# Kernel tuning notes

Hardware: AMD Instinct MI355X
Metric: run time of the kernel (lower is better)

The kernel has to match this reference:

```python
import jax, jax.numpy as jnp
import numpy as np

B = 32768      # number of sets
N = 131072     # total elements
DIM = 128      # feature dim
HID = 64       # hidden dim
MAXP = 17      # max_n + 1 (one-hot positional dim / size-class count)


def _ln(x, g, b, eps=1e-5):
    m = jnp.mean(x, -1, keepdims=True)
    v = jnp.var(x, -1, keepdims=True)
    return (x - m) * jax.lax.rsqrt(v + eps) * g + b


def _mlp_ln(x, w1, b1, g, bt, w2, b2):
    return jnp.tanh(_ln(x @ w1 + b1, g, bt)) @ w2 + b2


def _mlp(x, w1, b1, w2, b2):
    return jnp.tanh(x @ w1 + b1) @ w2 + b2


def _lin_init(key, fan_in, fan_out):
    k1, k2 = jax.random.split(key)
    s = 1.0 / np.sqrt(fan_in)
    return (jax.random.uniform(k1, (fan_in, fan_out), jnp.float32, -s, s),
            jax.random.uniform(k2, (fan_out,), jnp.float32, -s, s))


def setup_inputs() -> dict:
    key = jax.random.key(0)
    ks = jax.random.split(key, 16)
    inp = {}
    inp['x'] = jax.random.normal(ks[0], (N, DIM), jnp.float32)
    inp['batch'] = jnp.sort(jax.random.randint(ks[1], (N,), 0, B)).astype(jnp.int64)
    # rank: Linear(dim, 1)
    inp['rank_w'], inp['rank_b'] = _lin_init(ks[2], DIM, 1)
    # enc_psi: dim -> 96 -> hid, LayerNorm
    inp['psi_w1'], inp['psi_b1'] = _lin_init(ks[3], DIM, 96)
    inp['psi_g'] = jnp.ones((96,), jnp.float32); inp['psi_bt'] = jnp.zeros((96,), jnp.float32)
    inp['psi_w2'], inp['psi_b2'] = _lin_init(ks[4], 96, HID)
    # encoder pos_encoder: 17 -> 40 -> hid, LayerNorm
    inp['pe_e_w1'], inp['pe_e_b1'] = _lin_init(ks[5], MAXP, 40)
    inp['pe_e_g'] = jnp.ones((40,), jnp.float32); inp['pe_e_bt'] = jnp.zeros((40,), jnp.float32)
    inp['pe_e_w2'], inp['pe_e_b2'] = _lin_init(ks[6], 40, HID)
    # enc_phi: (hid+17)=81 -> 72 -> hid, no LN
    inp['phi_w1'], inp['phi_b1'] = _lin_init(ks[7], HID + MAXP, 72)
    inp['phi_w2'], inp['phi_b2'] = _lin_init(ks[8], 72, HID)
    # size_pred: hid -> 40 -> 17, no LN
    inp['size_w1'], inp['size_b1'] = _lin_init(ks[9], HID, 40)
    inp['size_w2'], inp['size_b2'] = _lin_init(ks[10], 40, MAXP)
    # decoder pos_encoder: 17 -> 40 -> hid, LayerNorm
    inp['pe_d_w1'], inp['pe_d_b1'] = _lin_init(ks[11], MAXP, 40)
    inp['pe_d_g'] = jnp.ones((40,), jnp.float32); inp['pe_d_bt'] = jnp.zeros((40,), jnp.float32)
    inp['pe_d_w2'], inp['pe_d_b2'] = _lin_init(ks[12], 40, HID)
    # decoder: hid -> 96 -> dim, no LN
    inp['dec_w1'], inp['dec_b1'] = _lin_init(ks[13], HID, 96)
    inp['dec_w2'], inp['dec_b2'] = _lin_init(ks[14], 96, DIM)
    return inp


def reference(x, batch, rank_w, rank_b,
              psi_w1, psi_b1, psi_g, psi_bt, psi_w2, psi_b2,
              pe_e_w1, pe_e_b1, pe_e_g, pe_e_bt, pe_e_w2, pe_e_b2,
              phi_w1, phi_b1, phi_w2, phi_b2,
              size_w1, size_b1, size_w2, size_b2,
              pe_d_w1, pe_d_b1, pe_d_g, pe_d_bt, pe_d_w2, pe_d_b2,
              dec_w1, dec_b1, dec_w2, dec_b2):
    batch = batch.astype(jnp.int32)
    # ---- Encoder ----
    n = jax.ops.segment_sum(jnp.ones(N, jnp.int32), batch, num_segments=B)  # [B]
    seg_start = jnp.cumsum(n) - n                                           # ptr[:-1]
    mag = (x @ rank_w + rank_b).reshape(-1)                                 # rank scores
    idx = jnp.lexsort((mag, batch))  # per-segment sort (batch is grouped/sorted)
    xs = x[idx]                                                             # [N, DIM]
    keys = jnp.arange(N) - seg_start[batch]                                 # position in set
    pos = jax.nn.one_hot(keys, MAXP, dtype=x.dtype)                         # [N, MAXP]
    y1 = _mlp_ln(xs, psi_w1, psi_b1, psi_g, psi_bt, psi_w2, psi_b2) * \
         _mlp_ln(pos, pe_e_w1, pe_e_b1, pe_e_g, pe_e_bt, pe_e_w2, pe_e_b2)
    y2 = jax.ops.segment_sum(y1, batch, num_segments=B)                     # [B, HID]
    pos_n = jax.nn.one_hot(n, MAXP, dtype=x.dtype)
    z = _mlp(jnp.concatenate([y2, pos_n], -1), phi_w1, phi_b1, phi_w2, phi_b2)  # [B, HID]
    # ---- Decoder ----
    logits = _mlp(z, size_w1, size_b1, size_w2, size_b2)                    # [B, MAXP]
    n_dec = jnp.argmax(logits, -1)                                          # [B]
    pe = _mlp_ln(jnp.eye(MAXP, dtype=x.dtype),
                 pe_d_w1, pe_d_b1, pe_d_g, pe_d_bt, pe_d_w2, pe_d_b2)       # [MAXP, HID]
    zp = z[:, None, :] * pe[None, :, :]                                     # [B, MAXP, HID]
    xr = _mlp(zp, dec_w1, dec_b1, dec_w2, dec_b2)                           # [B, MAXP, DIM]
    mask = jnp.arange(MAXP)[None, :] < n_dec[:, None]                       # valid slots
    xr = jnp.where(mask[..., None], xr, 0.0)
    batchr = jnp.broadcast_to(jnp.arange(B)[:, None], (B, MAXP))
    return xr.reshape(B * MAXP, DIM), batchr.reshape(-1), mask.reshape(-1)
```

## Files before the change

### kernel.cpp

```cpp
#include <hip/hip_runtime.h>

#define NELEM 131072
#define BSETS 32768
#define DIM 128
#define HID 64
#define MAXP 17

typedef __attribute__((ext_vector_type(8))) short short8;
typedef __attribute__((ext_vector_type(4))) float f32x4;

__device__ __forceinline__ unsigned short f2bf(float f) {
  unsigned u = __float_as_uint(f);
  u += 0x7fff + ((u >> 16) & 1);
  return (unsigned short)(u >> 16);
}

__device__ void pos_mlp40(int row, const float* w1, const float* b1, const float* g,
                          const float* bt, const float* w2, const float* b2, float* out) {
  float h[40];
  for (int j = 0; j < 40; ++j) h[j] = b1[j] + (row >= 0 ? w1[row * 40 + j] : 0.0f);
  float s = 0.f;
  for (int j = 0; j < 40; ++j) s += h[j];
  float mean = s * (1.0f / 40.0f);
  float v = 0.f;
  for (int j = 0; j < 40; ++j) { float d = h[j] - mean; v += d * d; }
  float rs = rsqrtf(v * (1.0f / 40.0f) + 1e-5f);
  float tb[40];
  for (int j = 0; j < 40; ++j) tb[j] = tanhf((h[j] - mean) * rs * g[j] + bt[j]);
  for (int o = 0; o < 64; ++o) {
    float a = b2[o];
    for (int j = 0; j < 40; ++j) a += tb[j] * w2[j * 64 + o];
    out[o] = a;
  }
}

__global__ __launch_bounds__(256) void k_init(
    const float* __restrict__ x, const int* __restrict__ batch,
    const float* __restrict__ rank_w, const float* __restrict__ rank_b,
    double* __restrict__ mag, int* __restrict__ start,
    const float* ew1, const float* eb1, const float* eg, const float* ebt,
    const float* ew2, const float* eb2,
    const float* dw1, const float* db1, const float* dg, const float* dbt,
    const float* dw2, const float* db2,
    float* enc_tab, float* dec_tab,
    const float* __restrict__ decw1, const float* __restrict__ decw2,
    unsigned short* __restrict__ w1s, unsigned short* __restrict__ w2s) {
  int blk = blockIdx.x;
  int t = threadIdx.x;
  if (blk < 1024) {
    int lane = t & 63;
    int w = t >> 6;
    float2 wv = ((const float2*)rank_w)[lane];
    double w0 = wv.x, w1 = wv.y;
    double rb = rank_b[0];
    int rowbase = (blk * 4 + w) * 32;
    for (int it = 0; it < 32; ++it) {
      int row = rowbase + it;
      float2 xv = ((const float2*)(x + (size_t)row * DIM))[lane];
      double acc = (double)xv.x * w0 + (double)xv.y * w1;
#pragma unroll
      for (int m = 1; m < 64; m <<= 1)
        acc += __shfl_xor(acc, m, 64);
      if (lane == 0) mag[row] = acc + rb;
    }
  } else if (blk < 1536) {
    int i = (blk - 1024) * 256 + t;
    int b = batch[i];
    if (i == 0) {
      for (int bb = 0; bb <= b; ++bb) start[bb] = 0;
    } else {
      int bp = batch[i - 1];
      for (int bb = bp + 1; bb <= b; ++bb) start[bb] = i;
    }
    if (i == NELEM - 1) {
      for (int bb = b + 1; bb <= BSETS; ++bb) start[bb] = NELEM;
    }
  } else if (blk == 1536) {
    if (t < 18) {
      float out[64];
      pos_mlp40(t < 17 ? t : -1, ew1, eb1, eg, ebt, ew2, eb2, out);
      for (int o = 0; o < 64; ++o) enc_tab[t * 64 + o] = out[o];
    } else if (t >= 32 && t < 49) {
      float out[64];
      pos_mlp40(t - 32, dw1, db1, dg, dbt, dw2, db2, out);
      for (int o = 0; o < 64; ++o) dec_tab[(t - 32) * 64 + o] = out[o];
    }
  } else {
    int idx = (blk - 1537) * 256 + t;
    if (idx < 6144) {
      int i = idx & 7, lane = (idx >> 3) & 63, rest = idx >> 9;
      int jt = rest % 6, s = rest / 6;
      int k = s * 32 + (lane >> 4) * 8 + i;
      int n = jt * 16 + (lane & 15);
      w1s[idx] = f2bf(decw1[k * 96 + n]);
    }
    int idx2 = idx - 6144;
    if (idx2 >= 0 && idx2 < 12288) {
      int i = idx2 & 7, lane = (idx2 >> 3) & 63, rest = idx2 >> 9;
      int jt = rest % 8, s = rest / 8;
      int k = s * 32 + (lane >> 4) * 8 + i;
      int n = jt * 16 + (lane & 15);
      w2s[idx2] = f2bf(decw2[k * 128 + n]);
    }
  }
}

__global__ __launch_bounds__(256) void k_rank(const int* __restrict__ batch,
                                              const int* __restrict__ start,
                                              const double* __restrict__ mag,
                                              int* __restrict__ key) {
  int i = blockIdx.x * 256 + threadIdx.x;
  int b = batch[i];
  int s = start[b], e = start[b + 1];
  double mi = mag[i];
  int r = 0;
  for (int j = s; j < e; ++j) {
    double mj = mag[j];
    r += (mj < mi) || (mj == mi && j < i);
  }
  key[i] = r;
}

__global__ __launch_bounds__(256) void k_encoder(
    const float* __restrict__ x, const int* __restrict__ batch,
    const int* __restrict__ key, const int* __restrict__ start,
    const float* __restrict__ w1, const float* __restrict__ b1,
    const float* __restrict__ g, const float* __restrict__ bt,
    const float* __restrict__ w2, const float* __restrict__ b2,
    const float* __restrict__ enc_tab, float* __restrict__ y1) {
  __shared__ float xt[64][129];
  __shared__ float tt[64][97];
  __shared__ float ps1[4][64];
  __shared__ float ps2[4][64];
  int t = threadIdx.x;
  int base = blockIdx.x * 64;
  const float4* xg = (const float4*)(x + (size_t)base * DIM);
#pragma unroll
  for (int v = 0; v < 8; ++v) {
    int f = t + 256 * v;
    float4 val = xg[f];
    int e = f >> 5, kq = (f & 31) * 4;
    xt[e][kq] = val.x; xt[e][kq + 1] = val.y; xt[e][kq + 2] = val.z; xt[e][kq + 3] = val.w;
  }
  __syncthreads();
  int lane = t & 63;
  int w = __builtin_amdgcn_readfirstlane(t >> 6);
  int j0 = w * 24;
  float acc[24];
#pragma unroll
  for (int jj = 0; jj < 24; ++jj) acc[jj] = b1[j0 + jj];
  for (int k = 0; k < DIM; ++k) {
    float xv = xt[lane][k];
#pragma unroll
    for (int jj = 0; jj < 24; ++jj) acc[jj] += xv * w1[k * 96 + j0 + jj];
  }
  float s1 = 0.f, s2 = 0.f;
#pragma unroll
  for (int jj = 0; jj < 24; ++jj) { s1 += acc[jj]; s2 += acc[jj] * acc[jj]; }
  ps1[w][lane] = s1; ps2[w][lane] = s2;
  __syncthreads();
  float S1 = ps1[0][lane] + ps1[1][lane] + ps1[2][lane] + ps1[3][lane];
  float S2 = ps2[0][lane] + ps2[1][lane] + ps2[2][lane] + ps2[3][lane];
  float mean = S1 * (1.0f / 96.0f);
  float var = S2 * (1.0f / 96.0f) - mean * mean;
  float rs = rsqrtf(var + 1e-5f);
#pragma unroll
  for (int jj = 0; jj < 24; ++jj) {
    float hv = (acc[jj] - mean) * rs * g[j0 + jj] + bt[j0 + jj];
    tt[lane][j0 + jj] = tanhf(hv);
  }
  __syncthreads();
  int o0 = w * 16;
  float acc2[16];
#pragma unroll
  for (int oo = 0; oo < 16; ++oo) acc2[oo] = b2[o0 + oo];
  for (int j = 0; j < 96; ++j) {
    float tv = tt[lane][j];
#pragma unroll
    for (int oo = 0; oo < 16; ++oo) acc2[oo] += tv * w2[j * 64 + o0 + oo];
  }
  int gi = base + lane;
  int kk = key[gi];
  int row = kk < MAXP ? kk : MAXP;
  int bb = batch[gi];
  int pos = start[bb] + kk;
  const float* pe = enc_tab + row * 64;
#pragma unroll
  for (int oo = 0; oo < 16; ++oo) acc2[oo] *= pe[o0 + oo];
  float4* d4 = (float4*)(y1 + (size_t)pos * 64 + o0);
#pragma unroll
  for (int q = 0; q < 4; ++q)
    d4[q] = make_float4(acc2[4 * q], acc2[4 * q + 1], acc2[4 * q + 2], acc2[4 * q + 3]);
}

__global__ __launch_bounds__(256) void k_phi(const float* __restrict__ y1,
                                             const int* __restrict__ start,
                                             const float* __restrict__ w1, const float* __restrict__ b1,
                                             const float* __restrict__ w2, const float* __restrict__ b2,
                                             const float* __restrict__ sw1, const float* __restrict__ sb1,
                                             const float* __restrict__ sw2, const float* __restrict__ sb2,
                                             float* __restrict__ z, int* __restrict__ ndec) {
  __shared__ float yt[64][65];
  __shared__ float tt[64][73];
  __shared__ float zt[64][65];
  __shared__ float st[64][41];
  int t = threadIdx.x;
  int base = blockIdx.x * 64;
  {
    int s = t >> 2, c = t & 3;
    int sb = base + s;
    int ps = start[sb], pe = start[sb + 1];
    float acc[16];
#pragma unroll
    for (int i = 0; i < 16; ++i) acc[i] = 0.f;
    for (int p = ps; p < pe; ++p) {
      const float4* row = (const float4*)(y1 + (size_t)p * 64 + c * 16);
#pragma unroll
      for (int q = 0; q < 4; ++q) {
        float4 v = row[q];
        acc[4 * q] += v.x; acc[4 * q + 1] += v.y; acc[4 * q + 2] += v.z; acc[4 * q + 3] += v.w;
      }
    }
#pragma unroll
    for (int i = 0; i < 16; ++i) yt[s][c * 16 + i] = acc[i];
  }
  __syncthreads();
  int lane = t & 63;
  int w = __builtin_amdgcn_readfirstlane(t >> 6);
  int sb = base + lane;
  int nb = start[sb + 1] - start[sb];
  int j0 = w * 18;
  float acc[18];
#pragma unroll
  for (int jj = 0; jj < 18; ++jj) acc[jj] = b1[j0 + jj];
  for (int k = 0; k < 64; ++k) {
    float yv = yt[lane][k];
#pragma unroll
    for (int jj = 0; jj < 18; ++jj) acc[jj] += yv * w1[k * 72 + j0 + jj];
  }
  if (nb < MAXP) {
    const float* wr = w1 + (64 + nb) * 72 + j0;
#pragma unroll
    for (int jj = 0; jj < 18; ++jj) acc[jj] += wr[jj];
  }
#pragma unroll
  for (int jj = 0; jj < 18; ++jj) tt[lane][j0 + jj] = tanhf(acc[jj]);
  __syncthreads();
  int o0 = w * 16;
  float acc2[16];
#pragma unroll
  for (int oo = 0; oo < 16; ++oo) acc2[oo] = b2[o0 + oo];
  for (int j = 0; j < 72; ++j) {
    float tv = tt[lane][j];
#pragma unroll
    for (int oo = 0; oo < 16; ++oo) acc2[oo] += tv * w2[j * 64 + o0 + oo];
  }
  float4* zd = (float4*)(z + (size_t)sb * 64 + o0);
#pragma unroll
  for (int q = 0; q < 4; ++q)
    zd[q] = make_float4(acc2[4 * q], acc2[4 * q + 1], acc2[4 * q + 2], acc2[4 * q + 3]);
#pragma unroll
  for (int oo = 0; oo < 16; ++oo) zt[lane][o0 + oo] = acc2[oo];
  __syncthreads();
  int s0 = w * 10;
  float hs[10];
#pragma unroll
  for (int jj = 0; jj < 10; ++jj) hs[jj] = sb1[s0 + jj];
  for (int o = 0; o < 64; ++o) {
    float v = zt[lane][o];
#pragma unroll
    for (int jj = 0; jj < 10; ++jj) hs[jj] += v * sw1[o * 40 + s0 + jj];
  }
#pragma unroll
  for (int jj = 0; jj < 10; ++jj) st[lane][s0 + jj] = tanhf(hs[jj]);
  __syncthreads();
  if (w == 0) {
    float lg[17];
#pragma unroll
    for (int l = 0; l < 17; ++l) lg[l] = sb2[l];
    for (int j = 0; j < 40; ++j) {
      float tv = st[lane][j];
#pragma unroll
      for (int l = 0; l < 17; ++l) lg[l] += tv * sw2[j * 17 + l];
    }
    float best = lg[0]; int bi = 0;
#pragma unroll
    for (int l = 1; l < 17; ++l) if (lg[l] > best) { best = lg[l]; bi = l; }
    ndec[sb] = bi;
  }
}

__global__ __launch_bounds__(256) void k_decoder(
    const float* __restrict__ z, const float* __restrict__ dec_tab,
    const unsigned short* __restrict__ w1s, const unsigned short* __restrict__ w2s,
    const float* __restrict__ b1, const float* __restrict__ b2,
    const int* __restrict__ ndec, float* __restrict__ out0,
    float* __restrict__ out1, float* __restrict__ out2) {
  __shared__ __align__(16) unsigned short h2[64][104];
  int t = threadIdx.x;
  int lane = t & 63;
  int w = __builtin_amdgcn_readfirstlane(t >> 6);
  int quad = lane >> 4, m = lane & 15;
  int r = blockIdx.x * 64 + w * 16 + m;
  int b = r / 17, p = r - b * 17;
  const float* zr = z + (size_t)b * 64;
  const float* per = dec_tab + p * 64;
  short8 a1[2];
#pragma unroll
  for (int s = 0; s < 2; ++s) {
    int k0 = s * 32 + quad * 8;
#pragma unroll
    for (int i = 0; i < 8; ++i) {
      float v = zr[k0 + i] * per[k0 + i];
      ((unsigned short*)&a1[s])[i] = f2bf(v);
    }
  }
  const short8* w1f = (const short8*)w1s;
  f32x4 acc[6] = {};
#pragma unroll
  for (int jt = 0; jt < 6; ++jt) {
    acc[jt] = __builtin_amdgcn_mfma_f32_16x16x32_bf16(a1[0], w1f[jt * 64 + lane], acc[jt], 0, 0, 0);
    acc[jt] = __builtin_amdgcn_mfma_f32_16x16x32_bf16(a1[1], w1f[(6 + jt) * 64 + lane], acc[jt], 0, 0, 0);
  }
#pragma unroll
  for (int jt = 0; jt < 6; ++jt) {
    int col = jt * 16 + m;
    float bias = b1[col];
#pragma unroll
    for (int reg = 0; reg < 4; ++reg) {
      int rl = w * 16 + quad * 4 + reg;
      h2[rl][col] = f2bf(tanhf(acc[jt][reg] + bias));
    }
  }
  __syncthreads();
  short8 a2[3];
#pragma unroll
  for (int s = 0; s < 3; ++s)
    a2[s] = *(const short8*)&h2[w * 16 + m][s * 32 + quad * 8];
  const short8* w2f = (const short8*)w2s;
  f32x4 acc2[8] = {};
#pragma unroll
  for (int nt = 0; nt < 8; ++nt) {
#pragma unroll
    for (int s = 0; s < 3; ++s)
      acc2[nt] = __builtin_amdgcn_mfma_f32_16x16x32_bf16(a2[s], w2f[(s * 8 + nt) * 64 + lane], acc2[nt], 0, 0, 0);
  }
#pragma unroll
  for (int nt = 0; nt < 8; ++nt) {
    int n = nt * 16 + m;
    float bias = b2[n];
#pragma unroll
    for (int reg = 0; reg < 4; ++reg) {
      int rl = w * 16 + quad * 4 + reg;
      int rg = blockIdx.x * 64 + rl;
      int bb = rg / 17, pp = rg - bb * 17;
      float v = acc2[nt][reg] + bias;
      if (pp >= ndec[bb]) v = 0.0f;
      out0[(size_t)rg * 128 + n] = v;
    }
  }
  if (t < 64) {
    int rg = blockIdx.x * 64 + t;
    int bb = rg / 17, pp = rg - bb * 17;
    out1[rg] = (float)bb;
    out2[rg] = (pp < ndec[bb]) ? 1.0f : 0.0f;
  }
}

extern "C" void kernel_launch(void* const* d_in, const int* in_sizes, int n_in,
                              void* d_out, int out_size, void* d_ws, size_t ws_size,
                              hipStream_t stream) {
  const float* x = (const float*)d_in[0];
  const int* batch = (const int*)d_in[1];
  const float* rank_w = (const float*)d_in[2];
  const float* rank_b = (const float*)d_in[3];
  const float* psi_w1 = (const float*)d_in[4];
  const float* psi_b1 = (const float*)d_in[5];
  const float* psi_g = (const float*)d_in[6];
  const float* psi_bt = (const float*)d_in[7];
  const float* psi_w2 = (const float*)d_in[8];
  const float* psi_b2 = (const float*)d_in[9];
  const float* pe_e_w1 = (const float*)d_in[10];
  const float* pe_e_b1 = (const float*)d_in[11];
  const float* pe_e_g = (const float*)d_in[12];
  const float* pe_e_bt = (const float*)d_in[13];
  const float* pe_e_w2 = (const float*)d_in[14];
  const float* pe_e_b2 = (const float*)d_in[15];
  const float* phi_w1 = (const float*)d_in[16];
  const float* phi_b1 = (const float*)d_in[17];
  const float* phi_w2 = (const float*)d_in[18];
  const float* phi_b2 = (const float*)d_in[19];
  const float* size_w1 = (const float*)d_in[20];
  const float* size_b1 = (const float*)d_in[21];
  const float* size_w2 = (const float*)d_in[22];
  const float* size_b2 = (const float*)d_in[23];
  const float* pe_d_w1 = (const float*)d_in[24];
  const float* pe_d_b1 = (const float*)d_in[25];
  const float* pe_d_g = (const float*)d_in[26];
  const float* pe_d_bt = (const float*)d_in[27];
  const float* pe_d_w2 = (const float*)d_in[28];
  const float* pe_d_b2 = (const float*)d_in[29];
  const float* dec_w1 = (const float*)d_in[30];
  const float* dec_b1 = (const float*)d_in[31];
  const float* dec_w2 = (const float*)d_in[32];
  const float* dec_b2 = (const float*)d_in[33];

  char* ws = (char*)d_ws;
  int* start = (int*)(ws);
  double* mag = (double*)(ws + 0x40000);
  int* key = (int*)(ws + 0x140000);
  float* enc_tab = (float*)(ws + 0x1C0000);
  float* dec_tab = (float*)(ws + 0x1C2000);
  unsigned short* w1s = (unsigned short*)(ws + 0x1C4000);
  unsigned short* w2s = (unsigned short*)(ws + 0x1C8000);
  float* zbuf = (float*)(ws + 0x200000);
  int* ndec = (int*)(ws + 0xA00000);

  float* out0 = (float*)d_out;
  float* out1 = out0 + 71303168;
  float* out2 = out1 + 557056;

  float* y1 = out0;

  k_init<<<1609, 256, 0, stream>>>(x, batch, rank_w, rank_b, mag, start,
                                   pe_e_w1, pe_e_b1, pe_e_g, pe_e_bt, pe_e_w2, pe_e_b2,
                                   pe_d_w1, pe_d_b1, pe_d_g, pe_d_bt, pe_d_w2, pe_d_b2,
                                   enc_tab, dec_tab, dec_w1, dec_w2, w1s, w2s);
  k_rank<<<512, 256, 0, stream>>>(batch, start, mag, key);
  k_encoder<<<2048, 256, 0, stream>>>(x, batch, key, start, psi_w1, psi_b1, psi_g, psi_bt,
                                      psi_w2, psi_b2, enc_tab, y1);
  k_phi<<<512, 256, 0, stream>>>(y1, start, phi_w1, phi_b1, phi_w2, phi_b2,
                                 size_w1, size_b1, size_w2, size_b2, zbuf, ndec);
  k_decoder<<<8704, 256, 0, stream>>>(zbuf, dec_tab, w1s, w2s, dec_b1, dec_b2, ndec,
                                      out0, out1, out2);
}
```

Baseline: 652.8 us.

## Fuse rank into encoder, use fast tanh, vectorize decoder input loads

Removes the separate k_rank launch and computes each element's within-set rank inside k_encoder, overlapping it with the x tile load and dropping the key buffer round trip. Replaces tanhf everywhere with an exp/reciprocal approximation. Merges the encoder's two shared-memory tiles into one aliased buffer to cut LDS use. Vectorizes the decoder's z*pe input loads with float4. The approximate tanh may change results slightly, and the exp form could give NaN for large inputs where exp overflows.

```diff
diff --git a/kernel.cpp b/kernel.cpp
--- a/kernel.cpp
+++ b/kernel.cpp
@@ -13,6 +13,12 @@
   unsigned u = __float_as_uint(f);
   u += 0x7fff + ((u >> 16) & 1);
   return (unsigned short)(u >> 16);
+}
+
+__device__ __forceinline__ float fast_tanh(float x) {
+  float t = __expf(2.0f * x);
+  float r = __builtin_amdgcn_rcpf(t + 1.0f);
+  return fmaf(-2.0f, r, 1.0f);
 }
 
 __device__ void pos_mlp40(int row, const float* w1, const float* b1, const float* g,
@@ -26,7 +32,7 @@
   for (int j = 0; j < 40; ++j) { float d = h[j] - mean; v += d * d; }
   float rs = rsqrtf(v * (1.0f / 40.0f) + 1e-5f);
   float tb[40];
-  for (int j = 0; j < 40; ++j) tb[j] = tanhf((h[j] - mean) * rs * g[j] + bt[j]);
+  for (int j = 0; j < 40; ++j) tb[j] = fast_tanh((h[j] - mean) * rs * g[j] + bt[j]);
   for (int o = 0; o < 64; ++o) {
     float a = b2[o];
     for (int j = 0; j < 40; ++j) a += tb[j] * w2[j * 64 + o];
@@ -105,31 +111,14 @@
   }
 }
 
-__global__ __launch_bounds__(256) void k_rank(const int* __restrict__ batch,
-                                              const int* __restrict__ start,
-                                              const double* __restrict__ mag,
-                                              int* __restrict__ key) {
-  int i = blockIdx.x * 256 + threadIdx.x;
-  int b = batch[i];
-  int s = start[b], e = start[b + 1];
-  double mi = mag[i];
-  int r = 0;
-  for (int j = s; j < e; ++j) {
-    double mj = mag[j];
-    r += (mj < mi) || (mj == mi && j < i);
-  }
-  key[i] = r;
-}
-
 __global__ __launch_bounds__(256) void k_encoder(
     const float* __restrict__ x, const int* __restrict__ batch,
-    const int* __restrict__ key, const int* __restrict__ start,
+    const double* __restrict__ mag, const int* __restrict__ start,
     const float* __restrict__ w1, const float* __restrict__ b1,
     const float* __restrict__ g, const float* __restrict__ bt,
     const float* __restrict__ w2, const float* __restrict__ b2,
     const float* __restrict__ enc_tab, float* __restrict__ y1) {
-  __shared__ float xt[64][129];
-  __shared__ float tt[64][97];
+  __shared__ float sm[64 * 129];
   __shared__ float ps1[4][64];
   __shared__ float ps2[4][64];
   int t = threadIdx.x;
@@ -140,17 +129,27 @@
     int f = t + 256 * v;
     float4 val = xg[f];
     int e = f >> 5, kq = (f & 31) * 4;
-    xt[e][kq] = val.x; xt[e][kq + 1] = val.y; xt[e][kq + 2] = val.z; xt[e][kq + 3] = val.w;
-  }
-  __syncthreads();
+    float* xr = sm + e * 129 + kq;
+    xr[0] = val.x; xr[1] = val.y; xr[2] = val.z; xr[3] = val.w;
+  }
   int lane = t & 63;
   int w = __builtin_amdgcn_readfirstlane(t >> 6);
+  int gi = base + lane;
+  int bseg = batch[gi];
+  int segs = start[bseg], sege = start[bseg + 1];
+  double mi = mag[gi];
+  int kk = 0;
+  for (int j = segs; j < sege; ++j) {
+    double mj = mag[j];
+    kk += (mj < mi) || (mj == mi && j < gi);
+  }
+  __syncthreads();
   int j0 = w * 24;
   float acc[24];
 #pragma unroll
   for (int jj = 0; jj < 24; ++jj) acc[jj] = b1[j0 + jj];
   for (int k = 0; k < DIM; ++k) {
-    float xv = xt[lane][k];
+    float xv = sm[lane * 129 + k];
 #pragma unroll
     for (int jj = 0; jj < 24; ++jj) acc[jj] += xv * w1[k * 96 + j0 + jj];
   }
@@ -167,7 +166,7 @@
 #pragma unroll
   for (int jj = 0; jj < 24; ++jj) {
     float hv = (acc[jj] - mean) * rs * g[j0 + jj] + bt[j0 + jj];
-    tt[lane][j0 + jj] = tanhf(hv);
+    sm[lane * 97 + j0 + jj] = fast_tanh(hv);
   }
   __syncthreads();
   int o0 = w * 16;
@@ -175,15 +174,12 @@
 #pragma unroll
   for (int oo = 0; oo < 16; ++oo) acc2[oo] = b2[o0 + oo];
   for (int j = 0; j < 96; ++j) {
-    float tv = tt[lane][j];
+    float tv = sm[lane * 97 + j];
 #pragma unroll
     for (int oo = 0; oo < 16; ++oo) acc2[oo] += tv * w2[j * 64 + o0 + oo];
   }
-  int gi = base + lane;
-  int kk = key[gi];
   int row = kk < MAXP ? kk : MAXP;
-  int bb = batch[gi];
-  int pos = start[bb] + kk;
+  int pos = segs + kk;
   const float* pe = enc_tab + row * 64;
 #pragma unroll
   for (int oo = 0; oo < 16; ++oo) acc2[oo] *= pe[o0 + oo];
@@ -244,7 +240,7 @@
     for (int jj = 0; jj < 18; ++jj) acc[jj] += wr[jj];
   }
 #pragma unroll
-  for (int jj = 0; jj < 18; ++jj) tt[lane][j0 + jj] = tanhf(acc[jj]);
+  for (int jj = 0; jj < 18; ++jj) tt[lane][j0 + jj] = fast_tanh(acc[jj]);
   __syncthreads();
   int o0 = w * 16;
   float acc2[16];
@@ -272,7 +268,7 @@
     for (int jj = 0; jj < 10; ++jj) hs[jj] += v * sw1[o * 40 + s0 + jj];
   }
 #pragma unroll
-  for (int jj = 0; jj < 10; ++jj) st[lane][s0 + jj] = tanhf(hs[jj]);
+  for (int jj = 0; jj < 10; ++jj) st[lane][s0 + jj] = fast_tanh(hs[jj]);
   __syncthreads();
   if (w == 0) {
     float lg[17];
@@ -303,17 +299,19 @@
   int quad = lane >> 4, m = lane & 15;
   int r = blockIdx.x * 64 + w * 16 + m;
   int b = r / 17, p = r - b * 17;
-  const float* zr = z + (size_t)b * 64;
-  const float* per = dec_tab + p * 64;
+  const float4* z4 = (const float4*)(z + (size_t)b * 64);
+  const float4* p4 = (const float4*)(dec_tab + p * 64);
   short8 a1[2];
 #pragma unroll
   for (int s = 0; s < 2; ++s) {
-    int k0 = s * 32 + quad * 8;
-#pragma unroll
-    for (int i = 0; i < 8; ++i) {
-      float v = zr[k0 + i] * per[k0 + i];
-      ((unsigned short*)&a1[s])[i] = f2bf(v);
-    }
+    int q0 = (s * 32 + quad * 8) >> 2;
+    float4 za = z4[q0], zb = z4[q0 + 1];
+    float4 pa = p4[q0], pb = p4[q0 + 1];
+    unsigned short* ap = (unsigned short*)&a1[s];
+    ap[0] = f2bf(za.x * pa.x); ap[1] = f2bf(za.y * pa.y);
+    ap[2] = f2bf(za.z * pa.z); ap[3] = f2bf(za.w * pa.w);
+    ap[4] = f2bf(zb.x * pb.x); ap[5] = f2bf(zb.y * pb.y);
+    ap[6] = f2bf(zb.z * pb.z); ap[7] = f2bf(zb.w * pb.w);
   }
   const short8* w1f = (const short8*)w1s;
   f32x4 acc[6] = {};
@@ -329,7 +327,7 @@
 #pragma unroll
     for (int reg = 0; reg < 4; ++reg) {
       int rl = w * 16 + quad * 4 + reg;
-      h2[rl][col] = f2bf(tanhf(acc[jt][reg] + bias));
+      h2[rl][col] = f2bf(fast_tanh(acc[jt][reg] + bias));
     }
   }
   __syncthreads();
@@ -408,7 +406,6 @@
   char* ws = (char*)d_ws;
   int* start = (int*)(ws);
   double* mag = (double*)(ws + 0x40000);
-  int* key = (int*)(ws + 0x140000);
   float* enc_tab = (float*)(ws + 0x1C0000);
   float* dec_tab = (float*)(ws + 0x1C2000);
   unsigned short* w1s = (unsigned short*)(ws + 0x1C4000);
@@ -426,8 +423,7 @@
                                    pe_e_w1, pe_e_b1, pe_e_g, pe_e_bt, pe_e_w2, pe_e_b2,
                                    pe_d_w1, pe_d_b1, pe_d_g, pe_d_bt, pe_d_w2, pe_d_b2,
                                    enc_tab, dec_tab, dec_w1, dec_w2, w1s, w2s);
-  k_rank<<<512, 256, 0, stream>>>(batch, start, mag, key);
-  k_encoder<<<2048, 256, 0, stream>>>(x, batch, key, start, psi_w1, psi_b1, psi_g, psi_bt,
+  k_encoder<<<2048, 256, 0, stream>>>(x, batch, mag, start, psi_w1, psi_b1, psi_g, psi_bt,
                                       psi_w2, psi_b2, enc_tab, y1);
   k_phi<<<512, 256, 0, stream>>>(y1, start, phi_w1, phi_b1, phi_w2, phi_b2,
                                  size_w1, size_b1, size_w2, size_b2, zbuf, ndec);
```

Result: faster. 627.1 us (-3.9%).
